# Performance work log

Measured on AMD Instinct MI355X. Metric: run time of the kernel, lower is better.

Reference implementation:

```python
import jax, jax.numpy as jnp
import numpy as np

B = 16
TOP_N = 4
IOU_THRESH = 0.25
PAD = 224
OUT = 224  # part image size
NUM_CLASSES = 200


def _gen_anchors(input_shape=(448, 448)):
    # Faithful port of NTSNet._generate_default_anchor_maps -> edge anchors,
    # then +PAD shift and int cast as in NTSNet.__init__.
    scales = [2.0 ** (1.0 / 3.0), 2.0 ** (2.0 / 3.0)]
    ratios = [0.667, 1.0, 1.5]
    settings = [(32, 48, scales), (64, 96, scales), (128, 192, [1.0] + scales)]
    edge = []
    for stride, size, scs in settings:
        H = int(np.ceil(input_shape[0] / stride))
        W = int(np.ceil(input_shape[1] / stride))
        ostart = stride / 2.0
        oy = np.arange(ostart, ostart + stride * H, stride).reshape(H, 1)
        ox = np.arange(ostart, ostart + stride * W, stride).reshape(1, W)
        cy = np.broadcast_to(oy, (H, W)).astype(np.float32)
        cx = np.broadcast_to(ox, (H, W)).astype(np.float32)
        for s in scs:
            for ar in ratios:
                h = size * s / float(ar) ** 0.5
                w = size * s * float(ar) ** 0.5
                e = np.stack([cy - h / 2.0, cx - w / 2.0, cy + h / 2.0, cx + w / 2.0], axis=-1)
                edge.append(e.reshape(-1, 4))
    edge = np.concatenate(edge, axis=0).astype(np.float32)
    return (edge + PAD).astype(np.int64).astype(np.int32)  # [1614,4] (y0,x0,y1,x1)


def _conv(x, w, b, stride, pad):
    y = jax.lax.conv_general_dilated(
        x, w, window_strides=(stride, stride),
        padding=[(pad, pad), (pad, pad)],
        dimension_numbers=("NCHW", "OIHW", "NCHW"))
    return y + b[None, :, None, None]


def _nms_single(scores, boxes, areas):
    # Hard NMS, fixed TOP_N iterations (jit-friendly): iteratively take the
    # highest-score box and suppress boxes with IoU >= IOU_THRESH.
    valid = jnp.ones(scores.shape, dtype=bool)
    picked = []
    for _ in range(TOP_N):
        i = jnp.argmax(jnp.where(valid, scores, -jnp.inf))
        b = boxes[i]
        ih = jnp.minimum(boxes[:, 2], b[2]) - jnp.maximum(boxes[:, 0], b[0])
        iw = jnp.minimum(boxes[:, 3], b[3]) - jnp.maximum(boxes[:, 1], b[1])
        inter = jnp.where((ih < 0) | (iw < 0), 0.0, ih * iw)
        iou = inter / (areas + areas[i] - inter)
        valid = valid & (iou < IOU_THRESH)
        picked.append(i)
    return jnp.stack(picked)  # [TOP_N]


def _crop_resize(img, box):
    # Bilinear resize of img[:, y0:y1, x0:x1] to OUTxOUT, align_corners=True
    # (matches F.interpolate(..., mode='bilinear', align_corners=True)).
    y0, x0, y1, x1 = box[0], box[1], box[2], box[3]
    h = (y1 - y0).astype(jnp.float32)
    w = (x1 - x0).astype(jnp.float32)
    t = jnp.arange(OUT, dtype=jnp.float32)
    sy = t * (h - 1.0) / (OUT - 1.0)
    sx = t * (w - 1.0) / (OUT - 1.0)
    fy = jnp.floor(sy)
    fx = jnp.floor(sx)
    wy = (sy - fy)[None, :, None]  # broadcast over rows
    wx = (sx - fx)[None, None, :]  # broadcast over cols
    iy0 = y0 + fy.astype(jnp.int32)
    ix0 = x0 + fx.astype(jnp.int32)
    iy1 = jnp.minimum(iy0 + 1, y1 - 1)
    ix1 = jnp.minimum(ix0 + 1, x1 - 1)
    r0 = img[:, iy0]  # [3,OUT,896]
    r1 = img[:, iy1]
    top = r0[:, :, ix0] * (1.0 - wx) + r0[:, :, ix1] * wx
    bot = r1[:, :, ix0] * (1.0 - wx) + r1[:, :, ix1] * wx
    return top * (1.0 - wy) + bot * wy  # [3,OUT,OUT]


def setup_inputs() -> dict:
    key = jax.random.key(0)
    ks = jax.random.split(key, 10)
    s = 0.02
    inp = {
        "x": jax.random.normal(ks[0], (B, 3, 448, 448), jnp.float32),
        "bb_w": jax.random.normal(ks[1], (2048, 3, 32, 32), jnp.float32) * s,
        "bb_b": jnp.zeros((2048,), jnp.float32),
        "n1_dw": jax.random.normal(ks[2], (128, 2048, 3, 3), jnp.float32) * s,
        "n1_db": jnp.zeros((128,), jnp.float32),
        "n1_tw": jax.random.normal(ks[3], (6, 128, 1, 1), jnp.float32) * s,
        "n1_tb": jnp.zeros((6,), jnp.float32),
        "n2_dw": jax.random.normal(ks[4], (128, 128, 3, 3), jnp.float32) * s,
        "n2_db": jnp.zeros((128,), jnp.float32),
        "n2_tw": jax.random.normal(ks[5], (6, 128, 1, 1), jnp.float32) * s,
        "n2_tb": jnp.zeros((6,), jnp.float32),
        "n3_dw": jax.random.normal(ks[6], (128, 128, 3, 3), jnp.float32) * s,
        "n3_db": jnp.zeros((128,), jnp.float32),
        "n3_tw": jax.random.normal(ks[7], (9, 128, 1, 1), jnp.float32) * s,
        "n3_tb": jnp.zeros((9,), jnp.float32),
        "cn_w": jax.random.normal(ks[8], (NUM_CLASSES, 10240), jnp.float32) * s,
        "cn_b": jnp.zeros((NUM_CLASSES,), jnp.float32),
        "anchors": jnp.asarray(_gen_anchors()),
    }
    return inp


def reference(x, bb_w, bb_b, n1_dw, n1_db, n1_tw, n1_tb, n2_dw, n2_db, n2_tw,
              n2_tb, n3_dw, n3_db, n3_tw, n3_tb, cn_w, cn_b, anchors):
    batch = x.shape[0]
    # Backbone -> raw pre-features [B,2048,14,14]
    raw = _conv(x, bb_w, bb_b, stride=32, pad=0)
    # Navigator unit -> rpn scores [B,1614]
    y1 = jax.nn.relu(_conv(raw, n1_dw, n1_db, 1, 1))            # [B,128,14,14]
    t1 = _conv(y1, n1_tw, n1_tb, 1, 0).reshape(batch, -1)        # [B,1176]
    y2 = jax.nn.relu(_conv(y1, n2_dw, n2_db, 2, 1))              # [B,128,7,7]
    t2 = _conv(y2, n2_tw, n2_tb, 1, 0).reshape(batch, -1)        # [B,294]
    y3 = jax.nn.relu(_conv(y2, n3_dw, n3_db, 2, 1))              # [B,128,4,4]
    t3 = _conv(y3, n3_tw, n3_tb, 1, 0).reshape(batch, -1)        # [B,144]
    rpn_score = jnp.concatenate([t1, t2, t3], axis=1)            # [B,1614]

    boxes_f = anchors.astype(jnp.float32)
    areas = (boxes_f[:, 2] - boxes_f[:, 0]) * (boxes_f[:, 3] - boxes_f[:, 1])
    top_idx = jax.vmap(_nms_single, in_axes=(0, None, None))(rpn_score, boxes_f, areas)  # [B,TOP_N]

    x_pad = jnp.pad(x, ((0, 0), (0, 0), (PAD, PAD), (PAD, PAD)))  # [B,3,896,896]
    sel_boxes = anchors[top_idx]                                  # [B,TOP_N,4]
    part_imgs = jax.vmap(lambda img, bs: jax.vmap(_crop_resize, in_axes=(None, 0))(img, bs))(
        x_pad, sel_boxes)                                         # [B,TOP_N,3,224,224]
    part_imgs = jax.lax.stop_gradient(part_imgs).reshape(batch * TOP_N, 3, OUT, OUT)

    # Shared backbone + tail (global avg pool; dropout is identity in eval)
    part_features = _conv(part_imgs, bb_w, bb_b, 32, 0).mean(axis=(2, 3))  # [B*TOP_N,2048]
    part_feature = part_features.reshape(batch, TOP_N, -1)[:, :4].reshape(batch, -1)  # num_cat=4
    raw_features = jax.lax.stop_gradient(raw).mean(axis=(2, 3))            # [B,2048]

    concat_out = jnp.concatenate([part_feature, raw_features], axis=1)     # [B,10240]
    concat_logits = concat_out @ cn_w.T + cn_b
    return concat_logits
```

## Files before the change

### kernel.cpp

```cpp
#include <hip/hip_runtime.h>
#include <cstdint>
#include <math.h>

typedef _Float16 half_t;
typedef __attribute__((ext_vector_type(8))) _Float16 half8;
typedef __attribute__((ext_vector_type(4))) float floatx4;


typedef __attribute__((address_space(3))) unsigned int lds_u32;
typedef const __attribute__((address_space(1))) unsigned int glb_u32;
__device__ __forceinline__ void glds16(const void* g, void* l) {
    __builtin_amdgcn_global_load_lds((glb_u32*)g, (lds_u32*)l, 16, 0, 0);
}

__global__ __launch_bounds__(256)
void prep_all(const float* __restrict__ x, const float* __restrict__ bbw,
              const float* __restrict__ n1dw, const float* __restrict__ n2dw,
              const float* __restrict__ n3dw, const float* __restrict__ cnb,
              const float* __restrict__ bbb,
              half_t* __restrict__ xh,
              half_t* __restrict__ bh, half_t* __restrict__ w1h,
              float* __restrict__ wt2t, float* __restrict__ wt3t,
              float* __restrict__ out, float* __restrict__ zpad,
              float* __restrict__ concat)
{
    const int t = blockIdx.x * 256 + threadIdx.x;
    if (t < 307200) {
        const int m = t % 3200, s = t / 3200;
        const int mt = m >> 7, mr = m & 127;
        float f[32];
        if (m < 3136) {
            const int bq = m / 196, pos = m % 196, oy = pos / 14, ox = pos % 14;
            const int c = s >> 5, r = s & 31;
            const float* p = x + ((size_t)(bq * 3 + c) * 448 + oy * 32 + r) * 448 + ox * 32;
            #pragma unroll
            for (int i = 0; i < 8; ++i) *(float4*)&f[i * 4] = *(const float4*)(p + i * 4);
        } else {
            #pragma unroll
            for (int j = 0; j < 32; ++j) f[j] = 0.f;
        }
        #pragma unroll
        for (int kg = 0; kg < 4; ++kg) {
            half8 h;
            #pragma unroll
            for (int j = 0; j < 8; ++j) h[j] = (half_t)f[kg * 8 + j];
            const size_t dst = (((size_t)(mt * 96 + s) * 4 + kg) * 128 + mr) * 8;
            *(half8*)(xh + dst) = h;
        }
    } else if (t < 503808) {
        const int t2 = t - 307200;
        const int n = t2 & 2047, s = t2 >> 11;
        const float* p = bbw + (size_t)n * 3072 + s * 32;
        float f[32];
        #pragma unroll
        for (int i = 0; i < 8; ++i) *(float4*)&f[i * 4] = *(const float4*)(p + i * 4);
        const int nt = n >> 6, nr = n & 63;
        #pragma unroll
        for (int kg = 0; kg < 4; ++kg) {
            half8 h;
            #pragma unroll
            for (int j = 0; j < 8; ++j) h[j] = (half_t)f[kg * 8 + j];
            const size_t dst = (((size_t)(nt * 96 + s) * 4 + kg) * 64 + nr) * 8;
            *(half8*)(bh + dst) = h;
        }
    } else if (t < 536576) {
        const int t2 = t - 503808;
        const int n = t2 >> 8, ic8 = t2 & 255;
        const int s = ic8 >> 2, kg = ic8 & 3;
        const float* src = n1dw + ((size_t)n * 2048 + ic8 * 8) * 9;
        float buf[72];
        #pragma unroll
        for (int i = 0; i < 18; ++i) *(float4*)&buf[i * 4] = *(const float4*)(src + i * 4);
        #pragma unroll
        for (int tap = 0; tap < 9; ++tap) {
            half8 h;
            #pragma unroll
            for (int j = 0; j < 8; ++j) h[j] = (half_t)buf[j * 9 + tap];
            const size_t dst = (((size_t)(tap * 64 + s) * 4 + kg) * 128 + n) * 8;
            *(half8*)(w1h + dst) = h;
        }
    } else if (t < 684032) {
        const int t2 = t - 536576;
        const int oc = t2 % 128, rest = t2 / 128, ic = rest % 128, tap = rest / 128;
        wt2t[(tap * 128 + ic) * 128 + oc] = n2dw[((size_t)oc * 128 + ic) * 9 + tap];
    } else if (t < 831488) {
        const int t2 = t - 684032;
        const int oc = t2 % 128, rest = t2 / 128, ic = rest % 128, tap = rest / 128;
        wt3t[(tap * 128 + ic) * 128 + oc] = n3dw[((size_t)oc * 128 + ic) * 9 + tap];
    } else if (t < 834688) {
        const int i = t - 831488;
        out[i] = cnb[i % 200];
    } else if (t < 834944) {
        zpad[t - 834688] = 0.f;
    } else if (t < 998784) {
        const int i = t - 834944;
        const int r = i % 10240;
        concat[i] = (r < 8192) ? bbb[r & 2047] : 0.f;
    }
}

__global__ __launch_bounds__(128)
void gemm_x(const half_t* __restrict__ Ah, const half_t* __restrict__ Bh,
            const float* __restrict__ bias, half_t* __restrict__ outh)
{
    __shared__ __align__(16) char L[32768];
    const int tid = threadIdx.x, lane = tid & 63, wv = tid >> 6;
    const int nt = blockIdx.x, mt = blockIdx.y;
    const int lm = lane & 15, quad = lane >> 4;

    const char* pA = (const char*)Ah + (size_t)(mt >> 1) * 786432
                   + quad * 2048 + ((mt & 1) * 64 + wv * 32 + lm) * 16;
    const char* gB = (const char*)Bh + (size_t)(2 * nt) * 393216 + lane * 16;

    floatx4 acc[2][8];
    const floatx4 fz = {0.f, 0.f, 0.f, 0.f};
    #pragma unroll
    for (int mi = 0; mi < 2; ++mi)
        #pragma unroll
        for (int j = 0; j < 8; ++j) acc[mi][j] = fz;

    half8 c0, c1, c2, c3, n0, n1, n2, n3;

    #pragma unroll
    for (int i = 0; i < 8; ++i)
        glds16(gB + (size_t)(i >> 2) * 393216 + (size_t)wv * 4096 + (i & 3) * 1024,
               L + wv * 8192 + i * 1024);
    c0 = *(const half8*)(pA);
    c1 = *(const half8*)(pA + 8192);
    c2 = *(const half8*)(pA + 256);
    c3 = *(const half8*)(pA + 8192 + 256);

    auto step = [&](int sn, const char* Lc, char* Ln,
                    half8& a00, half8& a01, half8& a10, half8& a11,
                    half8& b00, half8& b01, half8& b10, half8& b11) {
        #pragma unroll
        for (int i = 0; i < 8; ++i)
            glds16(gB + (size_t)(i >> 2) * 393216 + (size_t)(2 * sn + wv) * 4096 + (i & 3) * 1024,
                   Ln + wv * 8192 + i * 1024);
        const char* pAs = pA + (size_t)(2 * sn) * 8192;
        b00 = *(const half8*)(pAs);
        b01 = *(const half8*)(pAs + 8192);
        b10 = *(const half8*)(pAs + 256);
        b11 = *(const half8*)(pAs + 8192 + 256);
        asm volatile("s_waitcnt vmcnt(12)" ::: "memory");
        __builtin_amdgcn_s_barrier();
        __builtin_amdgcn_sched_barrier(0);
        #pragma unroll
        for (int ki = 0; ki < 2; ++ki) {
            const half8 a0 = ki ? a01 : a00;
            const half8 a1 = ki ? a11 : a10;
            #pragma unroll
            for (int j = 0; j < 8; ++j) {
                half8 b = *(const half8*)(Lc + ki * 8192 + (j >> 2) * 4096 + quad * 1024 + ((j & 3) * 16 + lm) * 16);
                acc[0][j] = __builtin_amdgcn_mfma_f32_16x16x32_f16(a0, b, acc[0][j], 0, 0, 0);
                acc[1][j] = __builtin_amdgcn_mfma_f32_16x16x32_f16(a1, b, acc[1][j], 0, 0, 0);
            }
        }
        __builtin_amdgcn_sched_barrier(0);
        __builtin_amdgcn_s_barrier();
    };

    for (int h = 0; h < 24; ++h) {
        const int s1 = 2 * h + 1;
        step(s1, L, L + 16384, c0, c1, c2, c3, n0, n1, n2, n3);
        step((s1 < 47) ? s1 + 1 : 0, L + 16384, L, n0, n1, n2, n3, c0, c1, c2, c3);
    }

    #pragma unroll
    for (int j = 0; j < 8; ++j) {
        const int n = nt * 128 + j * 16 + lm;
        const float bv = bias[n];
        #pragma unroll
        for (int mi = 0; mi < 2; ++mi) {
            const int m0 = mt * 64 + wv * 32 + mi * 16 + quad * 4;
            #pragma unroll
            for (int r = 0; r < 4; ++r)
                outh[(size_t)(m0 + r) * 2048 + n] = (half_t)(acc[mi][j][r] + bv);
        }
    }
}

__global__ __launch_bounds__(128)
void gemm_nav(const half_t* __restrict__ rawh, const half_t* __restrict__ Bh,
              const char* __restrict__ zpad, float* __restrict__ y1p)
{
    __shared__ __align__(16) char L[32768];
    const int tid = threadIdx.x, lane = tid & 63, wv = tid >> 6;
    const int tx = blockIdx.x;
    const int tap = tx >> 1, ks = tx & 1;
    const int mt = blockIdx.y;
    const int lm = lane & 15, quad = lane >> 4;

    const char* fb0; const char* fb1; int fs0, fs1;
    {
        const int g0 = mt * 64 + wv * 32 + lm;
        const int b = g0 / 196, pos = g0 % 196, oy = pos / 14, ox = pos % 14;
        const int iy = oy + tap / 3 - 1, ix = ox + tap % 3 - 1;
        const bool av = (iy >= 0 && iy < 14 && ix >= 0 && ix < 14);
        fb0 = av ? (const char*)rawh + ((size_t)(b * 196 + iy * 14 + ix)) * 4096 + ks * 2048 : zpad;
        fs0 = av ? 1 : 0;
    }
    {
        const int g1 = mt * 64 + wv * 32 + 16 + lm;
        const int b = g1 / 196, pos = g1 % 196, oy = pos / 14, ox = pos % 14;
        const int iy = oy + tap / 3 - 1, ix = ox + tap % 3 - 1;
        const bool av = (iy >= 0 && iy < 14 && ix >= 0 && ix < 14);
        fb1 = av ? (const char*)rawh + ((size_t)(b * 196 + iy * 14 + ix)) * 4096 + ks * 2048 : zpad;
        fs1 = av ? 1 : 0;
    }

    const char* gB = (const char*)Bh + (size_t)tap * 524288 + (size_t)(ks * 32) * 8192 + lane * 16;

    floatx4 acc[2][8];
    const floatx4 fz = {0.f, 0.f, 0.f, 0.f};
    #pragma unroll
    for (int mi = 0; mi < 2; ++mi)
        #pragma unroll
        for (int j = 0; j < 8; ++j) acc[mi][j] = fz;

    half8 c0, c1, c2, c3, n0, n1, n2, n3;

    #pragma unroll
    for (int i = 0; i < 8; ++i)
        glds16(gB + (size_t)wv * 8192 + i * 1024, L + wv * 8192 + i * 1024);
    c0 = *(const half8*)(fb0 + fs0 * (quad * 16));
    c1 = *(const half8*)(fb0 + fs0 * (64 + quad * 16));
    c2 = *(const half8*)(fb1 + fs1 * (quad * 16));
    c3 = *(const half8*)(fb1 + fs1 * (64 + quad * 16));

    auto step = [&](int sn, const char* Lc, char* Ln,
                    half8& a00, half8& a01, half8& a10, half8& a11,
                    half8& b00, half8& b01, half8& b10, half8& b11) {
        #pragma unroll
        for (int i = 0; i < 8; ++i)
            glds16(gB + (size_t)(2 * sn + wv) * 8192 + i * 1024, Ln + wv * 8192 + i * 1024);
        b00 = *(const half8*)(fb0 + fs0 * (sn * 128 + quad * 16));
        b01 = *(const half8*)(fb0 + fs0 * (sn * 128 + 64 + quad * 16));
        b10 = *(const half8*)(fb1 + fs1 * (sn * 128 + quad * 16));
        b11 = *(const half8*)(fb1 + fs1 * (sn * 128 + 64 + quad * 16));
        asm volatile("s_waitcnt vmcnt(12)" ::: "memory");
        __builtin_amdgcn_s_barrier();
        __builtin_amdgcn_sched_barrier(0);
        #pragma unroll
        for (int ki = 0; ki < 2; ++ki) {
            const half8 a0 = ki ? a01 : a00;
            const half8 a1 = ki ? a11 : a10;
            #pragma unroll
            for (int j = 0; j < 8; ++j) {
                half8 b = *(const half8*)(Lc + ki * 8192 + quad * 2048 + (j * 16 + lm) * 16);
                acc[0][j] = __builtin_amdgcn_mfma_f32_16x16x32_f16(a0, b, acc[0][j], 0, 0, 0);
                acc[1][j] = __builtin_amdgcn_mfma_f32_16x16x32_f16(a1, b, acc[1][j], 0, 0, 0);
            }
        }
        __builtin_amdgcn_sched_barrier(0);
        __builtin_amdgcn_s_barrier();
    };

    for (int h = 0; h < 8; ++h) {
        const int s1 = 2 * h + 1;
        step(s1, L, L + 16384, c0, c1, c2, c3, n0, n1, n2, n3);
        step((s1 < 15) ? s1 + 1 : 0, L + 16384, L, n0, n1, n2, n3, c0, c1, c2, c3);
    }

    #pragma unroll
    for (int j = 0; j < 8; ++j) {
        const int n = j * 16 + lm;
        #pragma unroll
        for (int mi = 0; mi < 2; ++mi) {
            const int m0 = mt * 64 + wv * 32 + mi * 16 + quad * 4;
            #pragma unroll
            for (int r = 0; r < 4; ++r)
                y1p[((size_t)tx * 3136 + m0 + r) * 128 + n] = acc[mi][j][r];
        }
    }
}

__global__ __launch_bounds__(256)
void y1r_rm(const float* __restrict__ y1p, const float* __restrict__ bias,
            float* __restrict__ y1,
            const half_t* __restrict__ rh, float* __restrict__ concat)
{
    if (blockIdx.x < 1568) {
        const int t = blockIdx.x * 256 + threadIdx.x;
        const int n = t & 127;
        float s = bias[n];
        #pragma unroll
        for (int ks = 0; ks < 18; ++ks) s += y1p[(size_t)ks * 3136 * 128 + t];
        y1[t] = fmaxf(s, 0.f);
    } else {
        const int t = (blockIdx.x - 1568) * 256 + threadIdx.x;
        const int n = t & 2047, b = (t >> 11) & 15, pc = t >> 15;
        float s = 0.f;
        const int p0 = pc * 49;
        for (int p = p0; p < p0 + 49; ++p)
            s += (float)rh[(size_t)(b * 196 + p) * 2048 + n];
        atomicAdd(concat + (size_t)b * 10240 + 8192 + n, s * (1.f / 196.f));
    }
}

__device__ __forceinline__ void tidy_one(const float* in, const float* wr, float bi,
                                         float* dst, int lane)
{
    float acc = in[lane] * wr[lane] + in[lane + 64] * wr[lane + 64];
    #pragma unroll
    for (int s = 32; s > 0; s >>= 1) acc += __shfl_down(acc, s, 64);
    if (lane == 0) *dst = acc + bi;
}

__device__ __forceinline__ void conv_s2_body(int t, const float* __restrict__ in,
                                             const float* __restrict__ wt,
                                             const float* __restrict__ bias,
                                             float* __restrict__ out, int Win, int Wout)
{
    const int oc = t & 127;
    const int pos = (t >> 7) % (Wout * Wout);
    const int b = t / (128 * Wout * Wout);
    if (b >= 16) return;
    const int oy = pos / Wout, ox = pos % Wout;
    float acc = bias[oc];
    for (int dy = 0; dy < 3; ++dy) {
        const int y = oy * 2 + dy - 1;
        if (y < 0 || y >= Win) continue;
        for (int dx = 0; dx < 3; ++dx) {
            const int x = ox * 2 + dx - 1;
            if (x < 0 || x >= Win) continue;
            const float* ip = in + (size_t)(b * Win * Win + y * Win + x) * 128;
            const float* wp = wt + (size_t)(dy * 3 + dx) * 16384 + oc;
            for (int ic = 0; ic < 128; ++ic)
                acc += ip[ic] * wp[ic * 128];
        }
    }
    out[(size_t)(b * Wout * Wout + pos) * 128 + oc] = fmaxf(acc, 0.f);
}

__global__ __launch_bounds__(256)
void conv2_tidy1(const float* __restrict__ y1, const float* __restrict__ wt2t,
                 const float* __restrict__ b2d, float* __restrict__ y2,
                 const float* __restrict__ w1t, const float* __restrict__ b1t,
                 float* __restrict__ scores)
{
    if (blockIdx.x < 392) {
        conv_s2_body(blockIdx.x * 256 + threadIdx.x, y1, wt2t, b2d, y2, 14, 7);
    } else {
        const int wid = (blockIdx.x - 392) * 4 + (threadIdx.x >> 6);
        const int lane = threadIdx.x & 63;
        if (wid >= 16 * 1176) return;
        const int b = wid / 1176, i1 = wid % 1176;
        const int ch = i1 / 196, pos = i1 % 196;
        tidy_one(y1 + (size_t)(b * 196 + pos) * 128, w1t + ch * 128, b1t[ch],
                 scores + b * 1614 + i1, lane);
    }
}

__global__ __launch_bounds__(256)
void conv3_tidy2(const float* __restrict__ y2, const float* __restrict__ wt3t,
                 const float* __restrict__ b3d, float* __restrict__ y3,
                 const float* __restrict__ w2t, const float* __restrict__ b2t,
                 float* __restrict__ scores)
{
    if (blockIdx.x < 128) {
        conv_s2_body(blockIdx.x * 256 + threadIdx.x, y2, wt3t, b3d, y3, 7, 4);
    } else {
        const int wid = (blockIdx.x - 128) * 4 + (threadIdx.x >> 6);
        const int lane = threadIdx.x & 63;
        if (wid >= 16 * 294) return;
        const int b = wid / 294, i2 = wid % 294;
        const int ch = i2 / 49, pos = i2 % 49;
        tidy_one(y2 + (size_t)(b * 49 + pos) * 128, w2t + ch * 128, b2t[ch],
                 scores + b * 1614 + 1176 + i2, lane);
    }
}

__global__ __launch_bounds__(256)
void tidy3(const float* __restrict__ y3, const float* __restrict__ w3t,
           const float* __restrict__ b3t, float* __restrict__ scores)
{
    const int wid = blockIdx.x * 4 + (threadIdx.x >> 6);
    const int lane = threadIdx.x & 63;
    if (wid >= 16 * 144) return;
    const int b = wid / 144, i3 = wid % 144;
    const int ch = i3 / 16, pos = i3 % 16;
    tidy_one(y3 + (size_t)(b * 16 + pos) * 128, w3t + ch * 128, b3t[ch],
             scores + b * 1614 + 1470 + i3, lane);
}

__global__ __launch_bounds__(256)
void nms(const float* __restrict__ scores, const int* __restrict__ anchors,
         int* __restrict__ top_idx)
{
    __shared__ float wv_v[4];
    __shared__ int wv_i[4];
    __shared__ int s_pick;
    const int b = blockIdx.x, tid = threadIdx.x;
    const int lane = tid & 63, wv = tid >> 6;
    float sc[7], ay0[7], ax0[7], ay1[7], ax1[7];
    unsigned int vmask = 0;
    #pragma unroll
    for (int j = 0; j < 7; ++j) {
        const int i = tid + j * 256;
        if (i < 1614) {
            sc[j]  = scores[b * 1614 + i];
            ay0[j] = (float)anchors[i * 4 + 0];
            ax0[j] = (float)anchors[i * 4 + 1];
            ay1[j] = (float)anchors[i * 4 + 2];
            ax1[j] = (float)anchors[i * 4 + 3];
            vmask |= 1u << j;
        }
    }
    for (int r = 0; r < 4; ++r) {
        float bv = -INFINITY; int bi = 0x7fffffff;
        #pragma unroll
        for (int j = 0; j < 7; ++j) {
            if (vmask & (1u << j)) {
                const float v = sc[j];
                const int i = tid + j * 256;
                if (v > bv || (v == bv && i < bi)) { bv = v; bi = i; }
            }
        }
        #pragma unroll
        for (int s = 32; s > 0; s >>= 1) {
            const float v2 = __shfl_down(bv, s, 64);
            const int   i2 = __shfl_down(bi, s, 64);
            if (v2 > bv || (v2 == bv && i2 < bi)) { bv = v2; bi = i2; }
        }
        if (lane == 0) { wv_v[wv] = bv; wv_i[wv] = bi; }
        __syncthreads();
        if (tid == 0) {
            float fv = wv_v[0]; int fi = wv_i[0];
            #pragma unroll
            for (int k = 1; k < 4; ++k)
                if (wv_v[k] > fv || (wv_v[k] == fv && wv_i[k] < fi)) { fv = wv_v[k]; fi = wv_i[k]; }
            s_pick = fi;
            top_idx[b * 4 + r] = fi;
        }
        __syncthreads();
        const int pick = s_pick;
        const float py0 = (float)anchors[pick * 4 + 0], px0 = (float)anchors[pick * 4 + 1];
        const float py1 = (float)anchors[pick * 4 + 2], px1 = (float)anchors[pick * 4 + 3];
        const float pa = (py1 - py0) * (px1 - px0);
        #pragma unroll
        for (int j = 0; j < 7; ++j) {
            if (vmask & (1u << j)) {
                const float ih = fminf(ay1[j], py1) - fmaxf(ay0[j], py0);
                const float iw = fminf(ax1[j], px1) - fmaxf(ax0[j], px0);
                const float inter = (ih < 0.f || iw < 0.f) ? 0.f : ih * iw;
                const float area = (ay1[j] - ay0[j]) * (ax1[j] - ax0[j]);
                const float iou = inter / ((area + pa) - inter);
                if (iou >= 0.25f) vmask &= ~(1u << j);
            }
        }
    }
}

__global__ __launch_bounds__(256)
void crop_mean(const float* __restrict__ x, const int* __restrict__ anchors,
               const int* __restrict__ top_idx, float* __restrict__ abar)
{
    __shared__ float red[256];
    const int bi = blockIdx.x;
    const int q = bi / 96, rem = bi % 96, c = rem >> 5, r = rem & 31;
    const int tid = threadIdx.x;
    const int cc = tid & 31, ps = tid >> 5;
    const int idx = top_idx[q];
    const int y0 = anchors[idx * 4 + 0], x0 = anchors[idx * 4 + 1];
    const int y1 = anchors[idx * 4 + 2], x1 = anchors[idx * 4 + 3];
    const float hh = (float)(y1 - y0), ww = (float)(x1 - x0);
    const float* xb = x + (size_t)((q >> 2) * 3 + c) * 200704;
    float acc = 0.f;
    for (int p = ps; p < 49; p += 8) {
        const int oy = p / 7, ox = p % 7;
        const int typ = oy * 32 + r;
        const int txp = ox * 32 + cc;
        const float sy = (float)typ * (hh - 1.0f) / 223.0f;
        const float fy = floorf(sy);
        const float wy = sy - fy;
        const int iy0 = y0 + (int)fy;
        const int iy1 = min(iy0 + 1, y1 - 1);
        const float sx = (float)txp * (ww - 1.0f) / 223.0f;
        const float fx = floorf(sx);
        const float wx = sx - fx;
        const int ix0 = x0 + (int)fx;
        const int ix1 = min(ix0 + 1, x1 - 1);
        const int ry0 = iy0 - 224, ry1 = iy1 - 224;
        const int rx0 = ix0 - 224, rx1 = ix1 - 224;
        const bool vy0 = (ry0 >= 0 && ry0 < 448), vy1 = (ry1 >= 0 && ry1 < 448);
        const bool vx0 = (rx0 >= 0 && rx0 < 448), vx1 = (rx1 >= 0 && rx1 < 448);
        const float v00 = (vy0 && vx0) ? xb[(size_t)ry0 * 448 + rx0] : 0.f;
        const float v01 = (vy0 && vx1) ? xb[(size_t)ry0 * 448 + rx1] : 0.f;
        const float v10 = (vy1 && vx0) ? xb[(size_t)ry1 * 448 + rx0] : 0.f;
        const float v11 = (vy1 && vx1) ? xb[(size_t)ry1 * 448 + rx1] : 0.f;
        const float top = v00 * (1.f - wx) + v01 * wx;
        const float bot = v10 * (1.f - wx) + v11 * wx;
        acc += top * (1.f - wy) + bot * wy;
    }
    red[tid] = acc;
    __syncthreads();
    if (tid < 32) {
        float s = 0.f;
        #pragma unroll
        for (int k = 0; k < 8; ++k) s += red[tid + 32 * k];
        abar[(size_t)q * 3072 + c * 1024 + r * 32 + cc] = s * (1.f / 49.f);
    }
}

__global__ __launch_bounds__(256)
void part_gemm(const float* __restrict__ abar, const half_t* __restrict__ Bh,
               float* __restrict__ concat)
{
    __shared__ __align__(16) char L[12288];
    const int tid = threadIdx.x, lane = tid & 63, wv = tid >> 6;
    const int lm = lane & 15, quad = lane >> 4;
    const int nt = blockIdx.x, ks = blockIdx.y;
    const char* gBh = (const char*)Bh + ((size_t)nt * 96 + ks * 12) * 4096 + lane * 16;
    const int am = tid & 63, akg = tid >> 6;

    floatx4 acc[4], accl[4];
    const floatx4 fz = {0.f, 0.f, 0.f, 0.f};
    #pragma unroll
    for (int j = 0; j < 4; ++j) { acc[j] = fz; accl[j] = fz; }

    for (int s = 0; s < 12; ++s) {
        {
            const float* pa = abar + (size_t)am * 3072 + (ks * 12 + s) * 32 + akg * 8;
            float f[8];
            *(float4*)&f[0] = *(const float4*)pa;
            *(float4*)&f[4] = *(const float4*)(pa + 4);
            half8 h, l;
            #pragma unroll
            for (int j = 0; j < 8; ++j) {
                const half_t hh = (half_t)f[j];
                h[j] = hh;
                l[j] = (half_t)(f[j] - (float)hh);
            }
            *(half8*)(L + (akg * 64 + am) * 16) = h;
            *(half8*)(L + 4096 + (akg * 64 + am) * 16) = l;
        }
        glds16(gBh + (size_t)s * 4096 + wv * 1024, L + 8192 + wv * 1024);
        __syncthreads();
        half8 ah, al, bh[4];
        ah = *(const half8*)(L + (quad * 64 + wv * 16 + lm) * 16);
        al = *(const half8*)(L + 4096 + (quad * 64 + wv * 16 + lm) * 16);
        #pragma unroll
        for (int j = 0; j < 4; ++j) bh[j] = *(const half8*)(L + 8192 + (quad * 64 + j * 16 + lm) * 16);
        #pragma unroll
        for (int j = 0; j < 4; ++j) {
            acc[j]  = __builtin_amdgcn_mfma_f32_16x16x32_f16(ah, bh[j], acc[j], 0, 0, 0);
            accl[j] = __builtin_amdgcn_mfma_f32_16x16x32_f16(al, bh[j], accl[j], 0, 0, 0);
        }
        __syncthreads();
    }
    #pragma unroll
    for (int j = 0; j < 4; ++j) {
        const int n = nt * 64 + j * 16 + lm;
        #pragma unroll
        for (int r = 0; r < 4; ++r) {
            const int m = wv * 16 + quad * 4 + r;
            atomicAdd(concat + (size_t)(m >> 2) * 10240 + (m & 3) * 2048 + n,
                      acc[j][r] + accl[j][r]);
        }
    }
}

__global__ __launch_bounds__(256)
void cls_gemm(const float* __restrict__ concat, const float* __restrict__ w,
              float* __restrict__ out)
{
    __shared__ float ws_[8 * 321];
    __shared__ float cs_[16 * 321];
    __shared__ float red[256];
    const int nchunk = blockIdx.x, ks = blockIdx.y;
    const int tid = threadIdx.x;
    for (int i = tid; i < 2560; i += 256) {
        const int r = i / 320, k = i % 320;
        ws_[r * 321 + k] = w[(size_t)(nchunk * 8 + r) * 10240 + ks * 320 + k];
    }
    for (int i = tid; i < 5120; i += 256) {
        const int r = i / 320, k = i % 320;
        cs_[r * 321 + k] = concat[(size_t)r * 10240 + ks * 320 + k];
    }
    __syncthreads();
    const int b = tid & 15, c = (tid >> 4) & 7, hf = tid >> 7;
    const float* cp = cs_ + b * 321 + hf * 160;
    const float* wp = ws_ + c * 321 + hf * 160;
    float a = 0.f;
    #pragma unroll 8
    for (int k = 0; k < 160; ++k) a += cp[k] * wp[k];
    red[tid] = a;
    __syncthreads();
    if (tid < 128) atomicAdd(out + b * 200 + nchunk * 8 + c, red[tid] + red[tid + 128]);
}

extern "C" void kernel_launch(void* const* d_in, const int* in_sizes, int n_in,
                              void* d_out, int out_size, void* d_ws, size_t ws_size,
                              hipStream_t stream)
{
    const float* x     = (const float*)d_in[0];
    const float* bb_w  = (const float*)d_in[1];
    const float* bb_b  = (const float*)d_in[2];
    const float* n1_dw = (const float*)d_in[3];
    const float* n1_db = (const float*)d_in[4];
    const float* n1_tw = (const float*)d_in[5];
    const float* n1_tb = (const float*)d_in[6];
    const float* n2_dw = (const float*)d_in[7];
    const float* n2_db = (const float*)d_in[8];
    const float* n2_tw = (const float*)d_in[9];
    const float* n2_tb = (const float*)d_in[10];
    const float* n3_dw = (const float*)d_in[11];
    const float* n3_db = (const float*)d_in[12];
    const float* n3_tw = (const float*)d_in[13];
    const float* n3_tb = (const float*)d_in[14];
    const float* cn_w  = (const float*)d_in[15];
    const float* cn_b  = (const float*)d_in[16];
    const int*   anchors = (const int*)d_in[17];
    float* out = (float*)d_out;
    char* W = (char*)d_ws;

    half_t* bbwh  = (half_t*)(W + 0);
    float*  zpad  = (float*)(W + 12582912);
    int*    topidx= (int*)(W + 12583936);
    float*  scores= (float*)(W + 12584960);
    float*  y1    = (float*)(W + 12688384);
    float*  y2    = (float*)(W + 14294016);
    float*  y3    = (float*)(W + 14695424);
    float*  concat= (float*)(W + 14826496);
    half_t* w1h   = (half_t*)(W + 15481856);
    float*  wt2t  = (float*)(W + 20200448);
    float*  wt3t  = (float*)(W + 20790272);
    char* E = W + 21380096;
    half_t* xh    = (half_t*)E;
    float*  y1p   = (float*)E;
    char* F = W + 60701696;
    half_t* rawh  = (half_t*)F;
    float*  abar  = (float*)F;

    prep_all<<<3902, 256, 0, stream>>>(x, bb_w, n1_dw, n2_dw, n3_dw, cn_b, bb_b,
                                       xh, bbwh, w1h, wt2t, wt3t, out, zpad, concat);

    gemm_x<<<dim3(16, 49), 128, 0, stream>>>(xh, bbwh, bb_b, rawh);
    gemm_nav<<<dim3(18, 49), 128, 0, stream>>>(rawh, w1h, (const char*)zpad, y1p);
    y1r_rm<<<2080, 256, 0, stream>>>(y1p, n1_db, y1, rawh, concat);

    conv2_tidy1<<<5096, 256, 0, stream>>>(y1, wt2t, n2_db, y2, n1_tw, n1_tb, scores);
    conv3_tidy2<<<1304, 256, 0, stream>>>(y2, wt3t, n3_db, y3, n2_tw, n2_tb, scores);
    tidy3<<<576, 256, 0, stream>>>(y3, n3_tw, n3_tb, scores);

    nms<<<16, 256, 0, stream>>>(scores, anchors, topidx);
    crop_mean<<<6144, 256, 0, stream>>>(x, anchors, topidx, abar);

    part_gemm<<<dim3(32, 8), 256, 0, stream>>>(abar, bbwh, concat);
    cls_gemm<<<dim3(25, 32), 256, 0, stream>>>(concat, cn_w, out);
}
```

Measured before the change: 372.2 us.

## Use four waves per block in backbone and navigator GEMMs with XCD-aware block remap

Both MFMA GEMM kernels move from 2 to 4 waves per block, splitting the 128-wide N tile between wave pairs so each wave holds half the accumulators. The cooperative LDS load of the B tile is divided among four waves. Block IDs are remapped so blocks landing on the same XCD share B columns (gemm_x) or contiguous tiles (gemm_nav), aiming for better L2 reuse. The extra waves raise latency hiding and occupancy. In exchange, each wave now loads its own copy of the A fragments, doubling redundant A global reads.

```diff
diff --git a/kernel.cpp b/kernel.cpp
--- a/kernel.cpp
+++ b/kernel.cpp
@@ -99,50 +99,56 @@
     }
 }
 
-__global__ __launch_bounds__(128)
+__global__ __launch_bounds__(256)
 void gemm_x(const half_t* __restrict__ Ah, const half_t* __restrict__ Bh,
             const float* __restrict__ bias, half_t* __restrict__ outh)
 {
     __shared__ __align__(16) char L[32768];
     const int tid = threadIdx.x, lane = tid & 63, wv = tid >> 6;
-    const int nt = blockIdx.x, mt = blockIdx.y;
+    const int bid = blockIdx.y * 16 + blockIdx.x;
+    const int xcd = bid & 7, ii = bid >> 3;
+    const int nt = 2 * xcd + (ii & 1), mt = ii >> 1;
     const int lm = lane & 15, quad = lane >> 4;
+    const int wr = wv >> 1, wc = wv & 1;
 
     const char* pA = (const char*)Ah + (size_t)(mt >> 1) * 786432
-                   + quad * 2048 + ((mt & 1) * 64 + wv * 32 + lm) * 16;
-    const char* gB = (const char*)Bh + (size_t)(2 * nt) * 393216 + lane * 16;
-
-    floatx4 acc[2][8];
+                   + quad * 2048 + ((mt & 1) * 64 + wr * 32 + lm) * 16;
+
+    const int kiw = wv >> 1, nhw = wv & 1;
+    const char* gBp = (const char*)Bh + (size_t)(2 * nt + nhw) * 393216 + lane * 16;
+    const int lB = kiw * 8192 + nhw * 4096;
+
+    const int brd = wc * 4096 + quad * 1024 + lm * 16;
+
+    floatx4 acc[2][4];
     const floatx4 fz = {0.f, 0.f, 0.f, 0.f};
     #pragma unroll
     for (int mi = 0; mi < 2; ++mi)
         #pragma unroll
-        for (int j = 0; j < 8; ++j) acc[mi][j] = fz;
-
-    half8 c0, c1, c2, c3, n0, n1, n2, n3;
-
-    #pragma unroll
-    for (int i = 0; i < 8; ++i)
-        glds16(gB + (size_t)(i >> 2) * 393216 + (size_t)wv * 4096 + (i & 3) * 1024,
-               L + wv * 8192 + i * 1024);
-    c0 = *(const half8*)(pA);
-    c1 = *(const half8*)(pA + 8192);
-    c2 = *(const half8*)(pA + 256);
-    c3 = *(const half8*)(pA + 8192 + 256);
+        for (int j = 0; j < 4; ++j) acc[mi][j] = fz;
+
+    half8 c00, c01, c10, c11, n00, n01, n10, n11;
+
+    #pragma unroll
+    for (int kg = 0; kg < 4; ++kg)
+        glds16(gBp + (size_t)kiw * 4096 + kg * 1024, L + lB + kg * 1024);
+    c00 = *(const half8*)(pA);
+    c01 = *(const half8*)(pA + 8192);
+    c10 = *(const half8*)(pA + 256);
+    c11 = *(const half8*)(pA + 8192 + 256);
 
     auto step = [&](int sn, const char* Lc, char* Ln,
                     half8& a00, half8& a01, half8& a10, half8& a11,
                     half8& b00, half8& b01, half8& b10, half8& b11) {
         #pragma unroll
-        for (int i = 0; i < 8; ++i)
-            glds16(gB + (size_t)(i >> 2) * 393216 + (size_t)(2 * sn + wv) * 4096 + (i & 3) * 1024,
-                   Ln + wv * 8192 + i * 1024);
-        const char* pAs = pA + (size_t)(2 * sn) * 8192;
+        for (int kg = 0; kg < 4; ++kg)
+            glds16(gBp + (size_t)(2 * sn + kiw) * 4096 + kg * 1024, Ln + lB + kg * 1024);
+        const char* pAs = pA + (size_t)sn * 16384;
         b00 = *(const half8*)(pAs);
         b01 = *(const half8*)(pAs + 8192);
         b10 = *(const half8*)(pAs + 256);
         b11 = *(const half8*)(pAs + 8192 + 256);
-        asm volatile("s_waitcnt vmcnt(12)" ::: "memory");
+        asm volatile("s_waitcnt vmcnt(8)" ::: "memory");
         __builtin_amdgcn_s_barrier();
         __builtin_amdgcn_sched_barrier(0);
         #pragma unroll
@@ -150,8 +156,8 @@
             const half8 a0 = ki ? a01 : a00;
             const half8 a1 = ki ? a11 : a10;
             #pragma unroll
-            for (int j = 0; j < 8; ++j) {
-                half8 b = *(const half8*)(Lc + ki * 8192 + (j >> 2) * 4096 + quad * 1024 + ((j & 3) * 16 + lm) * 16);
+            for (int j = 0; j < 4; ++j) {
+                half8 b = *(const half8*)(Lc + ki * 8192 + brd + j * 256);
                 acc[0][j] = __builtin_amdgcn_mfma_f32_16x16x32_f16(a0, b, acc[0][j], 0, 0, 0);
                 acc[1][j] = __builtin_amdgcn_mfma_f32_16x16x32_f16(a1, b, acc[1][j], 0, 0, 0);
             }
@@ -162,17 +168,17 @@
 
     for (int h = 0; h < 24; ++h) {
         const int s1 = 2 * h + 1;
-        step(s1, L, L + 16384, c0, c1, c2, c3, n0, n1, n2, n3);
-        step((s1 < 47) ? s1 + 1 : 0, L + 16384, L, n0, n1, n2, n3, c0, c1, c2, c3);
-    }
-
-    #pragma unroll
-    for (int j = 0; j < 8; ++j) {
-        const int n = nt * 128 + j * 16 + lm;
+        step(s1, L, L + 16384, c00, c01, c10, c11, n00, n01, n10, n11);
+        step((s1 < 47) ? s1 + 1 : 0, L + 16384, L, n00, n01, n10, n11, c00, c01, c10, c11);
+    }
+
+    #pragma unroll
+    for (int j = 0; j < 4; ++j) {
+        const int n = nt * 128 + wc * 64 + j * 16 + lm;
         const float bv = bias[n];
         #pragma unroll
         for (int mi = 0; mi < 2; ++mi) {
-            const int m0 = mt * 64 + wv * 32 + mi * 16 + quad * 4;
+            const int m0 = mt * 64 + wr * 32 + mi * 16 + quad * 4;
             #pragma unroll
             for (int r = 0; r < 4; ++r)
                 outh[(size_t)(m0 + r) * 2048 + n] = (half_t)(acc[mi][j][r] + bv);
@@ -180,20 +186,23 @@
     }
 }
 
-__global__ __launch_bounds__(128)
+__global__ __launch_bounds__(256)
 void gemm_nav(const half_t* __restrict__ rawh, const half_t* __restrict__ Bh,
               const char* __restrict__ zpad, float* __restrict__ y1p)
 {
     __shared__ __align__(16) char L[32768];
     const int tid = threadIdx.x, lane = tid & 63, wv = tid >> 6;
-    const int tx = blockIdx.x;
+    const int bid = blockIdx.y * 18 + blockIdx.x;
+    const int xcd = bid & 7, ii = bid >> 3;
+    const int Lx = (xcd < 2 ? xcd * 111 : 222 + (xcd - 2) * 110) + ii;
+    const int tx = Lx / 49, mt = Lx % 49;
     const int tap = tx >> 1, ks = tx & 1;
-    const int mt = blockIdx.y;
     const int lm = lane & 15, quad = lane >> 4;
+    const int wr = wv >> 1, wc = wv & 1;
 
     const char* fb0; const char* fb1; int fs0, fs1;
     {
-        const int g0 = mt * 64 + wv * 32 + lm;
+        const int g0 = mt * 64 + wr * 32 + lm;
         const int b = g0 / 196, pos = g0 % 196, oy = pos / 14, ox = pos % 14;
         const int iy = oy + tap / 3 - 1, ix = ox + tap % 3 - 1;
         const bool av = (iy >= 0 && iy < 14 && ix >= 0 && ix < 14);
@@ -201,7 +210,7 @@
         fs0 = av ? 1 : 0;
     }
     {
-        const int g1 = mt * 64 + wv * 32 + 16 + lm;
+        const int g1 = mt * 64 + wr * 32 + 16 + lm;
         const int b = g1 / 196, pos = g1 % 196, oy = pos / 14, ox = pos % 14;
         const int iy = oy + tap / 3 - 1, ix = ox + tap % 3 - 1;
         const bool av = (iy >= 0 && iy < 14 && ix >= 0 && ix < 14);
@@ -209,36 +218,43 @@
         fs1 = av ? 1 : 0;
     }
 
+    const int kiw = wv >> 1, kgh = wv & 1;
     const char* gB = (const char*)Bh + (size_t)tap * 524288 + (size_t)(ks * 32) * 8192 + lane * 16;
-
-    floatx4 acc[2][8];
+    int cof[4];
+    #pragma unroll
+    for (int t = 0; t < 4; ++t)
+        cof[t] = (kgh * 2 + (t >> 1)) * 2048 + (t & 1) * 1024;
+
+    const int brd = quad * 2048 + (wc * 64 + lm) * 16;
+
+    floatx4 acc[2][4];
     const floatx4 fz = {0.f, 0.f, 0.f, 0.f};
     #pragma unroll
     for (int mi = 0; mi < 2; ++mi)
         #pragma unroll
-        for (int j = 0; j < 8; ++j) acc[mi][j] = fz;
-
-    half8 c0, c1, c2, c3, n0, n1, n2, n3;
-
-    #pragma unroll
-    for (int i = 0; i < 8; ++i)
-        glds16(gB + (size_t)wv * 8192 + i * 1024, L + wv * 8192 + i * 1024);
-    c0 = *(const half8*)(fb0 + fs0 * (quad * 16));
-    c1 = *(const half8*)(fb0 + fs0 * (64 + quad * 16));
-    c2 = *(const half8*)(fb1 + fs1 * (quad * 16));
-    c3 = *(const half8*)(fb1 + fs1 * (64 + quad * 16));
+        for (int j = 0; j < 4; ++j) acc[mi][j] = fz;
+
+    half8 c00, c01, c10, c11, n00, n01, n10, n11;
+
+    #pragma unroll
+    for (int t = 0; t < 4; ++t)
+        glds16(gB + (size_t)kiw * 8192 + cof[t], L + kiw * 8192 + cof[t]);
+    c00 = *(const half8*)(fb0 + fs0 * (quad * 16));
+    c01 = *(const half8*)(fb0 + fs0 * (64 + quad * 16));
+    c10 = *(const half8*)(fb1 + fs1 * (quad * 16));
+    c11 = *(const half8*)(fb1 + fs1 * (64 + quad * 16));
 
     auto step = [&](int sn, const char* Lc, char* Ln,
                     half8& a00, half8& a01, half8& a10, half8& a11,
                     half8& b00, half8& b01, half8& b10, half8& b11) {
         #pragma unroll
-        for (int i = 0; i < 8; ++i)
-            glds16(gB + (size_t)(2 * sn + wv) * 8192 + i * 1024, Ln + wv * 8192 + i * 1024);
+        for (int t = 0; t < 4; ++t)
+            glds16(gB + (size_t)(2 * sn + kiw) * 8192 + cof[t], Ln + kiw * 8192 + cof[t]);
         b00 = *(const half8*)(fb0 + fs0 * (sn * 128 + quad * 16));
         b01 = *(const half8*)(fb0 + fs0 * (sn * 128 + 64 + quad * 16));
         b10 = *(const half8*)(fb1 + fs1 * (sn * 128 + quad * 16));
         b11 = *(const half8*)(fb1 + fs1 * (sn * 128 + 64 + quad * 16));
-        asm volatile("s_waitcnt vmcnt(12)" ::: "memory");
+        asm volatile("s_waitcnt vmcnt(8)" ::: "memory");
         __builtin_amdgcn_s_barrier();
         __builtin_amdgcn_sched_barrier(0);
         #pragma unroll
@@ -246,8 +262,8 @@
             const half8 a0 = ki ? a01 : a00;
             const half8 a1 = ki ? a11 : a10;
             #pragma unroll
-            for (int j = 0; j < 8; ++j) {
-                half8 b = *(const half8*)(Lc + ki * 8192 + quad * 2048 + (j * 16 + lm) * 16);
+            for (int j = 0; j < 4; ++j) {
+                half8 b = *(const half8*)(Lc + ki * 8192 + brd + j * 256);
                 acc[0][j] = __builtin_amdgcn_mfma_f32_16x16x32_f16(a0, b, acc[0][j], 0, 0, 0);
                 acc[1][j] = __builtin_amdgcn_mfma_f32_16x16x32_f16(a1, b, acc[1][j], 0, 0, 0);
             }
@@ -258,16 +274,16 @@
 
     for (int h = 0; h < 8; ++h) {
         const int s1 = 2 * h + 1;
-        step(s1, L, L + 16384, c0, c1, c2, c3, n0, n1, n2, n3);
-        step((s1 < 15) ? s1 + 1 : 0, L + 16384, L, n0, n1, n2, n3, c0, c1, c2, c3);
-    }
-
-    #pragma unroll
-    for (int j = 0; j < 8; ++j) {
-        const int n = j * 16 + lm;
+        step(s1, L, L + 16384, c00, c01, c10, c11, n00, n01, n10, n11);
+        step((s1 < 15) ? s1 + 1 : 0, L + 16384, L, n00, n01, n10, n11, c00, c01, c10, c11);
+    }
+
+    #pragma unroll
+    for (int j = 0; j < 4; ++j) {
+        const int n = wc * 64 + j * 16 + lm;
         #pragma unroll
         for (int mi = 0; mi < 2; ++mi) {
-            const int m0 = mt * 64 + wv * 32 + mi * 16 + quad * 4;
+            const int m0 = mt * 64 + wr * 32 + mi * 16 + quad * 4;
             #pragma unroll
             for (int r = 0; r < 4; ++r)
                 y1p[((size_t)tx * 3136 + m0 + r) * 128 + n] = acc[mi][j][r];
@@ -636,8 +652,8 @@
     prep_all<<<3902, 256, 0, stream>>>(x, bb_w, n1_dw, n2_dw, n3_dw, cn_b, bb_b,
                                        xh, bbwh, w1h, wt2t, wt3t, out, zpad, concat);
 
-    gemm_x<<<dim3(16, 49), 128, 0, stream>>>(xh, bbwh, bb_b, rawh);
-    gemm_nav<<<dim3(18, 49), 128, 0, stream>>>(rawh, w1h, (const char*)zpad, y1p);
+    gemm_x<<<dim3(16, 49), 256, 0, stream>>>(xh, bbwh, bb_b, rawh);
+    gemm_nav<<<dim3(18, 49), 256, 0, stream>>>(rawh, w1h, (const char*)zpad, y1p);
     y1r_rm<<<2080, 256, 0, stream>>>(y1p, n1_db, y1, rawh, concat);
 
     conv2_tidy1<<<5096, 256, 0, stream>>>(y1, wt2t, n2_db, y2, n1_tw, n1_tb, scores);
```

New measurement: 397.7 us. 6.8% more time.
